# Kernel tuning notes

Hardware: AMD Instinct MI355X
Metric: run time of the kernel (lower is better)

The kernel has to match this reference:

```python
import jax, jax.numpy as jnp
import numpy as np

N_NODES = 50000
N_EDGES = 800000
IN_DIM = 128
H_DIM = 128
NUM_RELS = 8


def setup_inputs() -> dict:
    key = jax.random.key(0)
    ks = jax.random.split(key, 10)
    s_in = 1.0 / np.sqrt(IN_DIM)
    s_h = 1.0 / np.sqrt(H_DIM)
    return {
        "features": jax.random.normal(ks[0], (N_NODES, IN_DIM), jnp.float32),
        "etypes": jax.random.randint(ks[1], (N_EDGES,), 0, NUM_RELS),
        "edge_weight": jax.random.uniform(ks[2], (N_EDGES,), jnp.float32),
        "src": jax.random.randint(ks[3], (N_EDGES,), 0, N_NODES),
        "dst": jax.random.randint(ks[4], (N_EDGES,), 0, N_NODES),
        "comp1": jax.random.normal(ks[5], (NUM_RELS, NUM_RELS), jnp.float32) * (1.0 / NUM_RELS),
        "V1": jax.random.normal(ks[6], (NUM_RELS, IN_DIM, H_DIM), jnp.float32) * s_in,
        "bias1": jnp.zeros((H_DIM,), jnp.float32),
        "comp2": jax.random.normal(ks[7], (NUM_RELS, NUM_RELS), jnp.float32) * (1.0 / NUM_RELS),
        "V2": jax.random.normal(ks[8], (NUM_RELS, H_DIM, H_DIM), jnp.float32) * s_h,
        "bias2": jnp.zeros((H_DIM,), jnp.float32),
    }


def _rel_graph_conv(x, src, dst, etypes, norm, comp, V, bias):
    # Basis decomposition: W[r] = sum_b comp[r,b] * V[b]  -> [R, in, out]
    W = jnp.einsum('rb,bio->rio', comp, V)
    # Transform every node by every relation once: [N, R, out]
    H = jnp.einsum('ni,rio->nro', x, W)
    # Per-edge message: gather (src, etype), scale by edge norm
    m = H[src, etypes] * norm  # [E, out]
    # Scatter-sum to destination nodes
    agg = jax.ops.segment_sum(m, dst, num_segments=x.shape[0])
    return agg + bias


def reference(features, etypes, edge_weight, src, dst,
              comp1, V1, bias1, comp2, V2, bias2):
    norm = edge_weight[:, None]  # edge_weight.unsqueeze(1)
    h = _rel_graph_conv(features, src, dst, etypes, norm, comp1, V1, bias1)
    h = jax.nn.relu(h)
    h = _rel_graph_conv(h, src, dst, etypes, norm, comp2, V2, bias2)
    # F.dropout with training=False is identity (eval mode)
    return h
```

## Files before the change

### kernel.cpp

```cpp
#include <hip/hip_runtime.h>
#include <stdint.h>

constexpr int N_NODES = 50000;
constexpr int N_EDGES = 800000;
constexpr int HD      = 128;
constexpr int NREL    = 8;
constexpr int NBUCK   = N_NODES * NREL;

typedef unsigned short ushortT;
using bf16x8 = __attribute__((ext_vector_type(8))) short;
using f32x4  = __attribute__((ext_vector_type(4))) float;

__device__ __forceinline__ float b2f(uint32_t lo16){
  uint32_t x = lo16 << 16; float f; __builtin_memcpy(&f,&x,4); return f;
}
__device__ __forceinline__ uint16_t f2b(float f){
  uint32_t x; __builtin_memcpy(&x,&f,4);
  uint32_t r = (x + 0x7FFFu + ((x>>16)&1u)) >> 16;
  return (uint16_t)r;
}

__global__ void k_zero2(int* __restrict__ a, int* __restrict__ b, int n){
  int i = blockIdx.x*blockDim.x + threadIdx.x;
  if(i<n){ a[i]=0; b[i]=0; }
}

__global__ void k_hist(const int* __restrict__ dst, const int* __restrict__ et,
                       int* __restrict__ deg){
  int i = blockIdx.x*blockDim.x + threadIdx.x;
  if(i<N_EDGES) atomicAdd(&deg[dst[i]*NREL + et[i]],1);
}

__global__ void k_scan1(const int* __restrict__ in, int* __restrict__ out,
                        int* __restrict__ part, int n){
  __shared__ int sm[256];
  int t = threadIdx.x; int i = blockIdx.x*256+t;
  int v = (i<n)? in[i] : 0;
  sm[t]=v; __syncthreads();
  for(int off=1; off<256; off<<=1){
    int x = (t>=off)? sm[t-off] : 0;
    __syncthreads();
    sm[t]+=x;
    __syncthreads();
  }
  if(i<n) out[i]=sm[t]-v;
  if(t==255) part[blockIdx.x]=sm[255];
}

__global__ void k_scan2(int* __restrict__ part, int nb){
  __shared__ int sm[256];
  int t=threadIdx.x;
  int v=(t<nb)? part[t] : 0;
  sm[t]=v; __syncthreads();
  for(int off=1; off<256; off<<=1){
    int x=(t>=off)? sm[t-off]:0;
    __syncthreads();
    sm[t]+=x;
    __syncthreads();
  }
  if(t<nb) part[t]=sm[t]-v;
}

__global__ void k_scan3(int* __restrict__ out, const int* __restrict__ part, int n){
  int i = blockIdx.x*blockDim.x+threadIdx.x;
  if(i<n) out[i]+=part[blockIdx.x];
}

__global__ void k_scatter(const int* __restrict__ src, const int* __restrict__ et,
                          const float* __restrict__ w, const int* __restrict__ dst,
                          const int* __restrict__ offs, int* __restrict__ cur,
                          int2* __restrict__ es){
  int i = blockIdx.x*blockDim.x + threadIdx.x;
  if(i<N_EDGES){
    int b = dst[i]*NREL + et[i];
    int pos = offs[b] + atomicAdd(&cur[b],1);
    int2 e; e.x = src[i]; e.y = __float_as_int(w[i]);
    es[pos] = e;
  }
}

__global__ void k_f2b(const float* __restrict__ in, ushortT* __restrict__ out, int n4){
  int i = blockIdx.x*blockDim.x + threadIdx.x;
  if(i<n4){
    float4 v = ((const float4*)in)[i];
    ushort4 o;
    o.x=f2b(v.x); o.y=f2b(v.y); o.z=f2b(v.z); o.w=f2b(v.w);
    ((ushort4*)out)[i]=o;
  }
}

__global__ void k_relw(const float* __restrict__ comp1, const float* __restrict__ V1,
                       const float* __restrict__ comp2, const float* __restrict__ V2,
                       ushortT* __restrict__ Wt1, ushortT* __restrict__ Wt2){
  int t = blockIdx.x*blockDim.x + threadIdx.x;
  int layer = t >> 17;
  t &= 131071;
  const float* comp = layer? comp2 : comp1;
  const float* V    = layer? V2    : V1;
  ushortT* Wt       = layer? Wt2   : Wt1;
  int o  = t >> 10;
  int rk = t & 1023;
  int r  = rk >> 7, k = rk & 127;
  float s=0.f;
  #pragma unroll
  for(int b=0;b<NREL;b++) s += comp[r*NREL+b]*V[(b<<14) + k*HD + o];
  Wt[t]=f2b(s);
}

__global__ void __launch_bounds__(256)
k_agg(const ushortT* __restrict__ xb,
      const int* __restrict__ offs, const int* __restrict__ deg,
      const int2* __restrict__ es,
      ushortT* __restrict__ Acat){
  int wave = blockIdx.x*4 + (threadIdx.x>>6);
  int lane = threadIdx.x & 63;
  int q = lane >> 4, f = lane & 15;
  int b = wave*4 + q;
  int beg = offs[b], cnt = deg[b];
  const int2* ep = es + beg;
  float a[8] = {};
  int2 e; e.x = 0; e.y = 0;
  if(cnt > 0) e = ep[0];
  for(int j=0;j<cnt;j++){
    int2 ce = e;
    if(j+1 < cnt) e = ep[j+1];
    float w = __int_as_float(ce.y);
    bf16x8 v = *(const bf16x8*)&xb[(size_t)ce.x*HD + f*8];
    #pragma unroll
    for(int t=0;t<8;t++) a[t] += w * b2f((uint16_t)v[t]);
  }
  uint32_t pk[4];
  #pragma unroll
  for(int i=0;i<4;i++)
    pk[i] = (uint32_t)f2b(a[2*i]) | ((uint32_t)f2b(a[2*i+1])<<16);
  *(uint4*)&Acat[(size_t)b*HD + f*8] = *(uint4*)pk;
}

constexpr int BM=64, BN=128, BK=64, LDK=72;
__global__ void __launch_bounds__(256)
k_gemm(const ushortT* __restrict__ A,
       const ushortT* __restrict__ Wt,
       const float* __restrict__ bias,
       float* __restrict__ outF,
       ushortT* __restrict__ outB,
       int M, int relu){
  __shared__ ushortT Asm[BM][LDK];
  __shared__ ushortT Bsm[BN][LDK];
  int tid = threadIdx.x;
  int wid = tid>>6, lane = tid&63;
  int l15 = lane&15, lhi = lane>>4;
  int row0 = blockIdx.x*BM;
  int wr = (wid>>1)*32, wc = (wid&1)*64;
  f32x4 acc[2][4] = {};
  for(int kt=0; kt<NREL*HD; kt+=BK){
    #pragma unroll
    for(int q=0;q<2;q++){
      int slot = q*256 + tid;
      int r = slot>>3, kb8 = (slot&7)*8;
      int grow = row0 + r; if(grow >= M) grow = M-1;
      *(bf16x8*)&Asm[r][kb8] = *(const bf16x8*)&A[(size_t)grow*1024 + kt + kb8];
    }
    #pragma unroll
    for(int q=0;q<4;q++){
      int slot = q*256 + tid;
      int c = slot>>3, kb8 = (slot&7)*8;
      *(bf16x8*)&Bsm[c][kb8] = *(const bf16x8*)&Wt[(size_t)c*1024 + kt + kb8];
    }
    __syncthreads();
    #pragma unroll
    for(int kk=0;kk<2;kk++){
      bf16x8 af[2], bfr[4];
      #pragma unroll
      for(int m=0;m<2;m++)  af[m]  = *(const bf16x8*)&Asm[wr + m*16 + l15][kk*32 + lhi*8];
      #pragma unroll
      for(int n=0;n<4;n++)  bfr[n] = *(const bf16x8*)&Bsm[wc + n*16 + l15][kk*32 + lhi*8];
      #pragma unroll
      for(int m=0;m<2;m++)
        #pragma unroll
        for(int n=0;n<4;n++)
          acc[m][n] = __builtin_amdgcn_mfma_f32_16x16x32_bf16(af[m], bfr[n], acc[m][n], 0,0,0);
    }
    __syncthreads();
  }
  #pragma unroll
  for(int m=0;m<2;m++){
    #pragma unroll
    for(int j=0;j<4;j++){
      int grow = row0 + wr + m*16 + lhi*4 + j;
      if(grow < M){
        #pragma unroll
        for(int n=0;n<4;n++){
          int col = wc + n*16 + l15;
          float v = acc[m][n][j] + bias[col];
          if(relu) v = fmaxf(v, 0.f);
          if(outF) outF[(size_t)grow*HD + col] = v;
          else     outB[(size_t)grow*HD + col] = f2b(v);
        }
      }
    }
  }
}

extern "C" void kernel_launch(void* const* d_in, const int* in_sizes, int n_in,
                              void* d_out, int out_size, void* d_ws, size_t ws_size,
                              hipStream_t stream){
  const float* feat  = (const float*)d_in[0];
  const int*   etyp  = (const int*)  d_in[1];
  const float* ew    = (const float*)d_in[2];
  const int*   src   = (const int*)  d_in[3];
  const int*   dst   = (const int*)  d_in[4];
  const float* comp1 = (const float*)d_in[5];
  const float* V1    = (const float*)d_in[6];
  const float* bias1 = (const float*)d_in[7];
  const float* comp2 = (const float*)d_in[8];
  const float* V2    = (const float*)d_in[9];
  const float* bias2 = (const float*)d_in[10];
  float* out = (float*)d_out;

  char* p = (char*)d_ws;
  auto alloc = [&](size_t bytes)->char* {
    char* q = p; p += (bytes + 255) & ~(size_t)255; return q;
  };
  ushortT* Wt1   = (ushortT*)alloc((size_t)HD*NREL*HD*2);
  ushortT* Wt2   = (ushortT*)alloc((size_t)HD*NREL*HD*2);
  ushortT* Acat  = (ushortT*)alloc((size_t)N_NODES*NREL*HD*2);
  ushortT* xb    = (ushortT*)alloc((size_t)N_NODES*HD*2);
  ushortT* hmid  = (ushortT*)alloc((size_t)N_NODES*HD*2);
  int*   deg   = (int*)  alloc((size_t)NBUCK*4);
  int*   offs  = (int*)  alloc((size_t)NBUCK*4);
  int*   cur   = (int*)  alloc((size_t)NBUCK*4);
  int*   part1 = (int*)  alloc(2048*4);
  int*   part2 = (int*)  alloc(256*4);
  int2*  es    = (int2*) alloc((size_t)N_EDGES*8);

  int zb = (NBUCK+255)/256;
  k_zero2<<<zb,256,0,stream>>>(deg,cur,NBUCK);
  k_hist<<<(N_EDGES+255)/256,256,0,stream>>>(dst,etyp,deg);
  int nb1 = (NBUCK+255)/256;
  int nb2 = (nb1+255)/256;
  k_scan1<<<nb1,256,0,stream>>>(deg,offs,part1,NBUCK);
  k_scan1<<<nb2,256,0,stream>>>(part1,part1,part2,nb1);
  k_scan2<<<1,256,0,stream>>>(part2,nb2);
  k_scan3<<<nb2,256,0,stream>>>(part1,part2,nb1);
  k_scan3<<<nb1,256,0,stream>>>(offs,part1,NBUCK);
  k_scatter<<<(N_EDGES+255)/256,256,0,stream>>>(src,etyp,ew,dst,offs,cur,es);

  int n4 = N_NODES*HD/4;
  k_f2b<<<(n4+255)/256,256,0,stream>>>(feat, xb, n4);
  k_relw<<<(2*HD*NREL*HD+255)/256,256,0,stream>>>(comp1,V1,comp2,V2,Wt1,Wt2);

  int aggGrid  = NBUCK/16;
  int gemmGrid = (N_NODES + BM - 1)/BM;
  k_agg<<<aggGrid,256,0,stream>>>(xb,   offs, deg, es, Acat);
  k_gemm<<<gemmGrid,256,0,stream>>>(Acat, Wt1, bias1, nullptr, hmid, N_NODES, 1);
  k_agg<<<aggGrid,256,0,stream>>>(hmid, offs, deg, es, Acat);
  k_gemm<<<gemmGrid,256,0,stream>>>(Acat, Wt2, bias2, out, nullptr, N_NODES, 0);
}
```

Before: 270.2 us.

## Pack edges into 32-bit records, drop LDS staging in GEMM, merge scan passes

```diff
diff --git a/kernel.cpp b/kernel.cpp
--- a/kernel.cpp
+++ b/kernel.cpp
@@ -1,4 +1,5 @@
 #include <hip/hip_runtime.h>
+#include <hip/hip_fp16.h>
 #include <stdint.h>
 
 constexpr int N_NODES = 50000;
@@ -47,18 +48,28 @@
   if(t==255) part[blockIdx.x]=sm[255];
 }
 
-__global__ void k_scan2(int* __restrict__ part, int nb){
+__global__ void k_scanmid(int* __restrict__ part, int n){
   __shared__ int sm[256];
+  __shared__ int carry;
   int t=threadIdx.x;
-  int v=(t<nb)? part[t] : 0;
-  sm[t]=v; __syncthreads();
-  for(int off=1; off<256; off<<=1){
-    int x=(t>=off)? sm[t-off]:0;
-    __syncthreads();
-    sm[t]+=x;
-    __syncthreads();
-  }
-  if(t<nb) part[t]=sm[t]-v;
+  if(t==0) carry=0;
+  __syncthreads();
+  for(int base=0; base<n; base+=256){
+    int i=base+t;
+    int v=(i<n)? part[i] : 0;
+    sm[t]=v; __syncthreads();
+    for(int off=1; off<256; off<<=1){
+      int x=(t>=off)? sm[t-off] : 0;
+      __syncthreads();
+      sm[t]+=x;
+      __syncthreads();
+    }
+    int tot = sm[255];
+    if(i<n) part[i]=sm[t]-v+carry;
+    __syncthreads();
+    if(t==0) carry += tot;
+    __syncthreads();
+  }
 }
 
 __global__ void k_scan3(int* __restrict__ out, const int* __restrict__ part, int n){
@@ -69,13 +80,14 @@
 __global__ void k_scatter(const int* __restrict__ src, const int* __restrict__ et,
                           const float* __restrict__ w, const int* __restrict__ dst,
                           const int* __restrict__ offs, int* __restrict__ cur,
-                          int2* __restrict__ es){
+                          uint32_t* __restrict__ es){
   int i = blockIdx.x*blockDim.x + threadIdx.x;
   if(i<N_EDGES){
     int b = dst[i]*NREL + et[i];
     int pos = offs[b] + atomicAdd(&cur[b],1);
-    int2 e; e.x = src[i]; e.y = __float_as_int(w[i]);
-    es[pos] = e;
+    __half h = __float2half(w[i]);
+    ushortT hb; __builtin_memcpy(&hb,&h,2);
+    es[pos] = (uint32_t)(src[i] & 0xFFFF) | ((uint32_t)hb << 16);
   }
 }
 
@@ -110,22 +122,25 @@
 __global__ void __launch_bounds__(256)
 k_agg(const ushortT* __restrict__ xb,
       const int* __restrict__ offs, const int* __restrict__ deg,
-      const int2* __restrict__ es,
+      const uint32_t* __restrict__ es,
       ushortT* __restrict__ Acat){
   int wave = blockIdx.x*4 + (threadIdx.x>>6);
   int lane = threadIdx.x & 63;
   int q = lane >> 4, f = lane & 15;
   int b = wave*4 + q;
   int beg = offs[b], cnt = deg[b];
-  const int2* ep = es + beg;
+  const uint32_t* ep = es + beg;
   float a[8] = {};
-  int2 e; e.x = 0; e.y = 0;
+  uint32_t e = 0;
   if(cnt > 0) e = ep[0];
   for(int j=0;j<cnt;j++){
-    int2 ce = e;
+    uint32_t ce = e;
     if(j+1 < cnt) e = ep[j+1];
-    float w = __int_as_float(ce.y);
-    bf16x8 v = *(const bf16x8*)&xb[(size_t)ce.x*HD + f*8];
+    ushortT hb = (ushortT)(ce >> 16);
+    __half h; __builtin_memcpy(&h,&hb,2);
+    float w = __half2float(h);
+    int s = (int)(ce & 0xFFFFu);
+    bf16x8 v = *(const bf16x8*)&xb[(size_t)s*HD + f*8];
     #pragma unroll
     for(int t=0;t<8;t++) a[t] += w * b2f((uint16_t)v[t]);
   }
@@ -136,7 +151,7 @@
   *(uint4*)&Acat[(size_t)b*HD + f*8] = *(uint4*)pk;
 }
 
-constexpr int BM=64, BN=128, BK=64, LDK=72;
+constexpr int BM=64;
 __global__ void __launch_bounds__(256)
 k_gemm(const ushortT* __restrict__ A,
        const ushortT* __restrict__ Wt,
@@ -144,43 +159,37 @@
        float* __restrict__ outF,
        ushortT* __restrict__ outB,
        int M, int relu){
-  __shared__ ushortT Asm[BM][LDK];
-  __shared__ ushortT Bsm[BN][LDK];
   int tid = threadIdx.x;
   int wid = tid>>6, lane = tid&63;
   int l15 = lane&15, lhi = lane>>4;
   int row0 = blockIdx.x*BM;
   int wr = (wid>>1)*32, wc = (wid&1)*64;
+  int r0 = row0 + wr + l15, r1 = r0 + 16;
+  if(r0 > M-1) r0 = M-1;
+  if(r1 > M-1) r1 = M-1;
+  const ushortT* Ap0 = A  + (size_t)r0*1024 + lhi*8;
+  const ushortT* Ap1 = A  + (size_t)r1*1024 + lhi*8;
+  const ushortT* Bp0 = Wt + (size_t)(wc     + l15)*1024 + lhi*8;
+  const ushortT* Bp1 = Wt + (size_t)(wc+16  + l15)*1024 + lhi*8;
+  const ushortT* Bp2 = Wt + (size_t)(wc+32  + l15)*1024 + lhi*8;
+  const ushortT* Bp3 = Wt + (size_t)(wc+48  + l15)*1024 + lhi*8;
   f32x4 acc[2][4] = {};
-  for(int kt=0; kt<NREL*HD; kt+=BK){
-    #pragma unroll
-    for(int q=0;q<2;q++){
-      int slot = q*256 + tid;
-      int r = slot>>3, kb8 = (slot&7)*8;
-      int grow = row0 + r; if(grow >= M) grow = M-1;
-      *(bf16x8*)&Asm[r][kb8] = *(const bf16x8*)&A[(size_t)grow*1024 + kt + kb8];
-    }
-    #pragma unroll
-    for(int q=0;q<4;q++){
-      int slot = q*256 + tid;
-      int c = slot>>3, kb8 = (slot&7)*8;
-      *(bf16x8*)&Bsm[c][kb8] = *(const bf16x8*)&Wt[(size_t)c*1024 + kt + kb8];
-    }
-    __syncthreads();
-    #pragma unroll
-    for(int kk=0;kk<2;kk++){
-      bf16x8 af[2], bfr[4];
-      #pragma unroll
-      for(int m=0;m<2;m++)  af[m]  = *(const bf16x8*)&Asm[wr + m*16 + l15][kk*32 + lhi*8];
-      #pragma unroll
-      for(int n=0;n<4;n++)  bfr[n] = *(const bf16x8*)&Bsm[wc + n*16 + l15][kk*32 + lhi*8];
-      #pragma unroll
-      for(int m=0;m<2;m++)
-        #pragma unroll
-        for(int n=0;n<4;n++)
-          acc[m][n] = __builtin_amdgcn_mfma_f32_16x16x32_bf16(af[m], bfr[n], acc[m][n], 0,0,0);
-    }
-    __syncthreads();
+  #pragma unroll 4
+  for(int kb=0; kb<32; kb++){
+    bf16x8 a0 = *(const bf16x8*)(Ap0 + kb*32);
+    bf16x8 a1 = *(const bf16x8*)(Ap1 + kb*32);
+    bf16x8 b0 = *(const bf16x8*)(Bp0 + kb*32);
+    bf16x8 b1 = *(const bf16x8*)(Bp1 + kb*32);
+    bf16x8 b2 = *(const bf16x8*)(Bp2 + kb*32);
+    bf16x8 b3 = *(const bf16x8*)(Bp3 + kb*32);
+    acc[0][0] = __builtin_amdgcn_mfma_f32_16x16x32_bf16(a0,b0,acc[0][0],0,0,0);
+    acc[0][1] = __builtin_amdgcn_mfma_f32_16x16x32_bf16(a0,b1,acc[0][1],0,0,0);
+    acc[0][2] = __builtin_amdgcn_mfma_f32_16x16x32_bf16(a0,b2,acc[0][2],0,0,0);
+    acc[0][3] = __builtin_amdgcn_mfma_f32_16x16x32_bf16(a0,b3,acc[0][3],0,0,0);
+    acc[1][0] = __builtin_amdgcn_mfma_f32_16x16x32_bf16(a1,b0,acc[1][0],0,0,0);
+    acc[1][1] = __builtin_amdgcn_mfma_f32_16x16x32_bf16(a1,b1,acc[1][1],0,0,0);
+    acc[1][2] = __builtin_amdgcn_mfma_f32_16x16x32_bf16(a1,b2,acc[1][2],0,0,0);
+    acc[1][3] = __builtin_amdgcn_mfma_f32_16x16x32_bf16(a1,b3,acc[1][3],0,0,0);
   }
   #pragma unroll
   for(int m=0;m<2;m++){
@@ -230,18 +239,14 @@
   int*   offs  = (int*)  alloc((size_t)NBUCK*4);
   int*   cur   = (int*)  alloc((size_t)NBUCK*4);
   int*   part1 = (int*)  alloc(2048*4);
-  int*   part2 = (int*)  alloc(256*4);
-  int2*  es    = (int2*) alloc((size_t)N_EDGES*8);
+  uint32_t* es = (uint32_t*)alloc((size_t)N_EDGES*4);
 
   int zb = (NBUCK+255)/256;
   k_zero2<<<zb,256,0,stream>>>(deg,cur,NBUCK);
   k_hist<<<(N_EDGES+255)/256,256,0,stream>>>(dst,etyp,deg);
   int nb1 = (NBUCK+255)/256;
-  int nb2 = (nb1+255)/256;
   k_scan1<<<nb1,256,0,stream>>>(deg,offs,part1,NBUCK);
-  k_scan1<<<nb2,256,0,stream>>>(part1,part1,part2,nb1);
-  k_scan2<<<1,256,0,stream>>>(part2,nb2);
-  k_scan3<<<nb2,256,0,stream>>>(part1,part2,nb1);
+  k_scanmid<<<1,256,0,stream>>>(part1,nb1);
   k_scan3<<<nb1,256,0,stream>>>(offs,part1,NBUCK);
   k_scatter<<<(N_EDGES+255)/256,256,0,stream>>>(src,etyp,ew,dst,offs,cur,es);
 
```

After: 394.2 us. 45.9% more time.
